# Kernel optimization log

Measured on AMD Instinct MI355X. Metric: run time of the kernel, lower is better.

## Reference

```python
import jax, jax.numpy as jnp
import numpy as np

DIM = 1024
HEADS = 16
SCALE = DIM ** (-0.5)  # NOTE: module scales by full dim, not head_dim


def setup_inputs() -> dict:
    key = jax.random.key(0)
    k1, k2, k3, k4 = jax.random.split(key, 4)
    x = jax.random.normal(k1, (4, 2048, DIM), dtype=jnp.float32)
    # torch Linear weights: y = x @ W.T
    w_qkv = jax.random.normal(k2, (3 * DIM, DIM), dtype=jnp.float32) * (DIM ** -0.5)
    w_out = jax.random.normal(k3, (DIM, DIM), dtype=jnp.float32) * (DIM ** -0.5)
    b_out = jax.random.normal(k4, (DIM,), dtype=jnp.float32) * 0.01
    return {"x": x, "w_qkv": w_qkv, "w_out": w_out, "b_out": b_out}


def reference(x, w_qkv, w_out, b_out):
    b, n, _ = x.shape
    h = HEADS
    d = DIM // h
    qkv = x @ w_qkv.T                                   # [b, n, 3*dim]
    qkv = qkv.reshape(b, n, 3, h, d)                    # split (qkv h d)
    qkv = jnp.transpose(qkv, (2, 0, 3, 1, 4))           # [3, b, h, n, d]
    q, k, v = qkv[0], qkv[1], qkv[2]
    dots = jnp.einsum('bhid,bhjd->bhij', q, k) * SCALE  # [b, h, n, n]
    attn = jax.nn.softmax(dots, axis=-1)
    out = jnp.einsum('bhij,bhjd->bhid', attn, v)        # [b, h, n, d]
    out = jnp.transpose(out, (0, 2, 1, 3)).reshape(b, n, h * d)
    return out @ w_out.T + b_out
```

## Files before the change

kernel.cpp:

```cpp
#include <hip/hip_runtime.h>

typedef short bf16x8 __attribute__((ext_vector_type(8)));
typedef float f32x4 __attribute__((ext_vector_type(4)));
typedef float f32x16 __attribute__((ext_vector_type(16)));

static __device__ __forceinline__ unsigned short f2bf(float f) {
  union { float f; unsigned u; } v; v.f = f;
  unsigned r = v.u + 0x7fffu + ((v.u >> 16) & 1u);
  return (unsigned short)(r >> 16);
}

static __device__ __forceinline__ unsigned pk2bf(float lo, float hi) {
  union { float f; unsigned u; } a, b; a.f = lo; b.f = hi;
  unsigned ra = a.u + 0x7fffu + ((a.u >> 16) & 1u);
  unsigned rb = b.u + 0x7fffu + ((b.u >> 16) & 1u);
  return __builtin_amdgcn_perm(rb, ra, 0x07060302);
}

static __device__ __forceinline__ void gll16(const unsigned short* g,
                                             unsigned short* l) {
  __builtin_amdgcn_global_load_lds(
      (const __attribute__((address_space(1))) unsigned int*)g,
      (__attribute__((address_space(3))) unsigned int*)l, 16, 0, 0);
}

__global__ void cvt_kernel(const float* __restrict__ src,
                           unsigned short* __restrict__ dst, int n4) {
  int i = blockIdx.x * blockDim.x + threadIdx.x;
  if (i >= n4) return;
  float4 f = ((const float4*)src)[i];
  ushort4 o;
  o.x = f2bf(f.x); o.y = f2bf(f.y); o.z = f2bf(f.z); o.w = f2bf(f.w);
  ((ushort4*)dst)[i] = o;
}

#define TM 128
#define TN 128
#define BK 64

template <int EPI>
__global__ __launch_bounds__(256, 2)
void gemm_bt(const unsigned short* __restrict__ X,
             const unsigned short* __restrict__ W,
             unsigned short* __restrict__ QKV, float* __restrict__ OUT,
             const float* __restrict__ bias, int M, int N, int K) {
  __shared__ __align__(16) unsigned short As[TM * BK];
  __shared__ __align__(16) unsigned short Bs[TN * BK];

  const int tid = threadIdx.x;
  const int lane = tid & 63;
  const int wave = tid >> 6;
  const int quad = lane >> 4;
  const int l16 = lane & 15;
  const int wm = wave >> 1, wn = wave & 1;

  const int m0 = blockIdx.y * TM;
  const int n0 = blockIdx.x * TN;

  const int sr = lane >> 3, sc = (lane & 7) * 8;

  f32x4 zero = {0.f, 0.f, 0.f, 0.f};
  f32x4 acc[4][4];
#pragma unroll
  for (int i = 0; i < 4; i++)
#pragma unroll
    for (int j = 0; j < 4; j++) acc[i][j] = zero;

  for (int k0 = 0; k0 < K; k0 += BK) {
    __syncthreads();
#pragma unroll
    for (int c = 0; c < 4; c++) {
      int row = wave * 32 + c * 8;
      gll16(&X[(size_t)(m0 + row + sr) * K + k0 + sc], &As[row * BK]);
      gll16(&W[(size_t)(n0 + row + sr) * K + k0 + sc], &Bs[row * BK]);
    }
    __syncthreads();
#pragma unroll
    for (int kk = 0; kk < 2; kk++) {
      bf16x8 af[4], bfr[4];
#pragma unroll
      for (int t = 0; t < 4; t++) {
        af[t]  = *(const bf16x8*)&As[(wm * 64 + t * 16 + l16) * BK + kk * 32 + quad * 8];
        bfr[t] = *(const bf16x8*)&Bs[(wn * 64 + t * 16 + l16) * BK + kk * 32 + quad * 8];
      }
#pragma unroll
      for (int mt = 0; mt < 4; mt++)
#pragma unroll
        for (int nt = 0; nt < 4; nt++)
          acc[mt][nt] = __builtin_amdgcn_mfma_f32_16x16x32_bf16(
              af[mt], bfr[nt], acc[mt][nt], 0, 0, 0);
    }
  }

#pragma unroll
  for (int mt = 0; mt < 4; mt++) {
#pragma unroll
    for (int nt = 0; nt < 4; nt++) {
      if (EPI == 0) {
        int nbase = n0 + wn * 64 + nt * 16;
        int which = nbase >> 10;
        if (which == 2) {
          int rem = (nbase + l16) & 1023;
          int h = rem >> 6, dd = rem & 63;
          int growb = m0 + wm * 64 + mt * 16 + quad * 4;
          int b = growb >> 11, nn0 = growb & 2047;
          ushort4 o;
          o.x = f2bf(acc[mt][nt][0]);
          o.y = f2bf(acc[mt][nt][1]);
          o.z = f2bf(acc[mt][nt][2]);
          o.w = f2bf(acc[mt][nt][3]);
          *(ushort4*)&QKV[16777216u + (((size_t)(b * 16 + h) * 64 + dd) << 11) + nn0] = o;
        } else {
#pragma unroll
          for (int r = 0; r < 4; r++) {
            int grow = m0 + wm * 64 + mt * 16 + quad * 4 + r;
            int gcol = nbase + l16;
            int rem = gcol & 1023;
            int h = rem >> 6, dd = rem & 63;
            float v = acc[mt][nt][r];
            if (which == 0) v *= 0.04508422f;
            int b = grow >> 11, nn = grow & 2047;
            QKV[(size_t)which * 8388608 +
                ((size_t)(b * 16 + h) * 2048 + nn) * 64 + dd] = f2bf(v);
          }
        }
      } else {
#pragma unroll
        for (int r = 0; r < 4; r++) {
          int grow = m0 + wm * 64 + mt * 16 + quad * 4 + r;
          int gcol = n0 + wn * 64 + nt * 16 + l16;
          OUT[(size_t)grow * N + gcol] = acc[mt][nt][r] + bias[gcol];
        }
      }
    }
  }
}

#define SK 72

__global__ __launch_bounds__(256, 2)
void attn_kernel(const unsigned short* __restrict__ Qg,
                 const unsigned short* __restrict__ Kg,
                 const unsigned short* __restrict__ Vg,
                 unsigned short* __restrict__ AO) {
  __shared__ __align__(16) unsigned short K_s[64 * SK];
  __shared__ __align__(16) unsigned short V_s[64 * SK];

  const int tid = threadIdx.x;
  const int lane = tid & 63;
  const int wave = tid >> 6;
  const int l31 = lane & 31;
  const int hh = lane >> 5;

  const int qb = blockIdx.x;
  const int bh = blockIdx.y;
  const size_t base = (size_t)bh * 131072;
  const int q0 = qb * 256 + wave * 64;

  bf16x8 bq[2][4];
#pragma unroll
  for (int mt = 0; mt < 2; mt++)
#pragma unroll
    for (int ks = 0; ks < 4; ks++)
      bq[mt][ks] = *(const bf16x8*)&Qg[base + (size_t)(q0 + mt * 32 + l31) * 64 +
                                       ks * 16 + hh * 8];

  f32x16 O[2][2];
#pragma unroll
  for (int mt = 0; mt < 2; mt++)
#pragma unroll
    for (int dt = 0; dt < 2; dt++)
#pragma unroll
      for (int r = 0; r < 16; r++) O[mt][dt][r] = 0.f;
  float lrow[2] = {0.f, 0.f};

  const int s_r = tid >> 3;
  const int s_c = (tid & 7) * 8;

  for (int j0 = 0; j0 < 2048; j0 += 64) {
    __syncthreads();
    *(uint4*)&K_s[s_r * SK + s_c] =
        *(const uint4*)&Kg[base + (size_t)(j0 + s_r) * 64 + s_c];
    *(uint4*)&K_s[(s_r + 32) * SK + s_c] =
        *(const uint4*)&Kg[base + (size_t)(j0 + s_r + 32) * 64 + s_c];
    *(uint4*)&V_s[s_r * SK + s_c] =
        *(const uint4*)&Vg[base + (size_t)s_r * 2048 + j0 + s_c];
    *(uint4*)&V_s[(s_r + 32) * SK + s_c] =
        *(const uint4*)&Vg[base + (size_t)(s_r + 32) * 2048 + j0 + s_c];
    __syncthreads();

    f32x16 S[2][2];
#pragma unroll
    for (int sub = 0; sub < 2; sub++) {
      f32x16 a0, a1;
#pragma unroll
      for (int r = 0; r < 16; r++) { a0[r] = 0.f; a1[r] = 0.f; }
#pragma unroll
      for (int ks = 0; ks < 4; ks++) {
        bf16x8 kf = *(const bf16x8*)&K_s[(sub * 32 + l31) * SK + ks * 16 + hh * 8];
        a0 = __builtin_amdgcn_mfma_f32_32x32x16_bf16(kf, bq[0][ks], a0, 0, 0, 0);
        a1 = __builtin_amdgcn_mfma_f32_32x32x16_bf16(kf, bq[1][ks], a1, 0, 0, 0);
      }
      S[sub][0] = a0; S[sub][1] = a1;
    }

#pragma unroll
    for (int mt = 0; mt < 2; mt++) {
      float rsum = 0.f;
#pragma unroll
      for (int sub = 0; sub < 2; sub++)
#pragma unroll
        for (int r = 0; r < 16; r++) {
          float p = __builtin_amdgcn_exp2f(S[sub][mt][r]);
          S[sub][mt][r] = p;
          rsum += p;
        }
      lrow[mt] += rsum;
    }

#pragma unroll
    for (int win = 0; win < 4; win++) {
      const int sub = win >> 1, kk = win & 1;
      const int g0 = kk * 2, g1 = kk * 2 + 1;
      bf16x8 pf[2];
#pragma unroll
      for (int mt = 0; mt < 2; mt++) {
        unsigned a00 = pk2bf(S[sub][mt][4 * g0 + 0], S[sub][mt][4 * g0 + 1]);
        unsigned a01 = pk2bf(S[sub][mt][4 * g0 + 2], S[sub][mt][4 * g0 + 3]);
        unsigned a10 = pk2bf(S[sub][mt][4 * g1 + 0], S[sub][mt][4 * g1 + 1]);
        unsigned a11 = pk2bf(S[sub][mt][4 * g1 + 2], S[sub][mt][4 * g1 + 3]);
        unsigned b00 = __shfl_xor((int)a00, 32);
        unsigned b01 = __shfl_xor((int)a01, 32);
        unsigned b10 = __shfl_xor((int)a10, 32);
        unsigned b11 = __shfl_xor((int)a11, 32);
        union { unsigned u[4]; bf16x8 v; } fr;
        fr.u[0] = hh ? b10 : a00;
        fr.u[1] = hh ? b11 : a01;
        fr.u[2] = hh ? a10 : b00;
        fr.u[3] = hh ? a11 : b01;
        pf[mt] = fr.v;
      }
#pragma unroll
      for (int dt = 0; dt < 2; dt++) {
        bf16x8 vf = *(const bf16x8*)&V_s[(dt * 32 + l31) * SK + win * 16 + hh * 8];
#pragma unroll
        for (int mt = 0; mt < 2; mt++)
          O[mt][dt] = __builtin_amdgcn_mfma_f32_32x32x16_bf16(vf, pf[mt], O[mt][dt], 0, 0, 0);
      }
    }
  }

  const int b4 = bh >> 4, head = bh & 15;
#pragma unroll
  for (int mt = 0; mt < 2; mt++) {
    lrow[mt] += __shfl_xor(lrow[mt], 32);
    float inv = 1.0f / lrow[mt];
    int row = b4 * 2048 + q0 + mt * 32 + l31;
#pragma unroll
    for (int dt = 0; dt < 2; dt++)
#pragma unroll
      for (int g = 0; g < 4; g++) {
        ushort4 o;
        o.x = f2bf(O[mt][dt][4 * g + 0] * inv);
        o.y = f2bf(O[mt][dt][4 * g + 1] * inv);
        o.z = f2bf(O[mt][dt][4 * g + 2] * inv);
        o.w = f2bf(O[mt][dt][4 * g + 3] * inv);
        *(ushort4*)&AO[(size_t)row * 1024 + head * 64 + dt * 32 + 8 * g + 4 * hh] = o;
      }
  }
}

extern "C" void kernel_launch(void* const* d_in, const int* in_sizes, int n_in,
                              void* d_out, int out_size, void* d_ws,
                              size_t ws_size, hipStream_t stream) {
  const float* x     = (const float*)d_in[0];
  const float* w_qkv = (const float*)d_in[1];
  const float* w_out = (const float*)d_in[2];
  const float* b_out = (const float*)d_in[3];
  float* out = (float*)d_out;

  unsigned short* ws = (unsigned short*)d_ws;
  unsigned short* Xbf  = ws;
  unsigned short* Wqkv = ws + 8388608;
  unsigned short* Wout = ws + 11534336;
  unsigned short* QKV  = ws + 12582912;
  unsigned short* AO   = ws;

  cvt_kernel<<<8192, 256, 0, stream>>>(x, Xbf, 2097152);
  cvt_kernel<<<3072, 256, 0, stream>>>(w_qkv, Wqkv, 786432);
  cvt_kernel<<<1024, 256, 0, stream>>>(w_out, Wout, 262144);

  gemm_bt<0><<<dim3(3072 / TN, 8192 / TM), 256, 0, stream>>>(
      Xbf, Wqkv, QKV, nullptr, nullptr, 8192, 3072, 1024);

  attn_kernel<<<dim3(8, 64), 256, 0, stream>>>(
      QKV, QKV + 8388608, QKV + 16777216, AO);

  gemm_bt<1><<<dim3(1024 / TN, 8192 / TM), 256, 0, stream>>>(
      AO, Wout, nullptr, out, b_out, 8192, 1024, 1024);
}
```

Measured before the change: 288.3 us.

## Swizzle LDS in GEMM and attention, double-buffer K/V with async loads

The GEMM's LDS tiles get an XOR column swizzle so that fragment reads spread across banks instead of conflicting. The attention kernel now double-buffers K/V tiles, filling them with global_load_lds prefetches of the next tile while the current one is computed. It also uses the same XOR swizzle in place of the padded layout. Each wave now owns 32 query rows instead of 64, the grid doubles and launch bounds ask for 4 blocks per CU, which raises occupancy but halves K/V reuse per block and doubles K/V global traffic. The loop keeps a single barrier per iteration; correctness depends on that barrier also covering completion of the previous async prefetch.

```diff
diff --git a/kernel.cpp b/kernel.cpp
--- a/kernel.cpp
+++ b/kernel.cpp
@@ -53,11 +53,13 @@
   const int quad = lane >> 4;
   const int l16 = lane & 15;
   const int wm = wave >> 1, wn = wave & 1;
+  const int rc = l16 & 7;
 
   const int m0 = blockIdx.y * TM;
   const int n0 = blockIdx.x * TN;
 
-  const int sr = lane >> 3, sc = (lane & 7) * 8;
+  const int sr = lane >> 3;
+  const int gsc = ((lane & 7) ^ sr) * 8;
 
   f32x4 zero = {0.f, 0.f, 0.f, 0.f};
   f32x4 acc[4][4];
@@ -71,17 +73,18 @@
 #pragma unroll
     for (int c = 0; c < 4; c++) {
       int row = wave * 32 + c * 8;
-      gll16(&X[(size_t)(m0 + row + sr) * K + k0 + sc], &As[row * BK]);
-      gll16(&W[(size_t)(n0 + row + sr) * K + k0 + sc], &Bs[row * BK]);
+      gll16(&X[(size_t)(m0 + row + sr) * K + k0 + gsc], &As[row * BK]);
+      gll16(&W[(size_t)(n0 + row + sr) * K + k0 + gsc], &Bs[row * BK]);
     }
     __syncthreads();
 #pragma unroll
     for (int kk = 0; kk < 2; kk++) {
       bf16x8 af[4], bfr[4];
+      const int csw = ((kk * 4 + quad) ^ rc) * 8;
 #pragma unroll
       for (int t = 0; t < 4; t++) {
-        af[t]  = *(const bf16x8*)&As[(wm * 64 + t * 16 + l16) * BK + kk * 32 + quad * 8];
-        bfr[t] = *(const bf16x8*)&Bs[(wn * 64 + t * 16 + l16) * BK + kk * 32 + quad * 8];
+        af[t]  = *(const bf16x8*)&As[(wm * 64 + t * 16 + l16) * BK + csw];
+        bfr[t] = *(const bf16x8*)&Bs[(wn * 64 + t * 16 + l16) * BK + csw];
       }
 #pragma unroll
       for (int mt = 0; mt < 4; mt++)
@@ -136,138 +139,128 @@
   }
 }
 
-#define SK 72
-
-__global__ __launch_bounds__(256, 2)
+__global__ __launch_bounds__(256, 4)
 void attn_kernel(const unsigned short* __restrict__ Qg,
                  const unsigned short* __restrict__ Kg,
                  const unsigned short* __restrict__ Vg,
                  unsigned short* __restrict__ AO) {
-  __shared__ __align__(16) unsigned short K_s[64 * SK];
-  __shared__ __align__(16) unsigned short V_s[64 * SK];
+  __shared__ __align__(16) unsigned short K_s[2][64 * 64];
+  __shared__ __align__(16) unsigned short V_s[2][64 * 64];
 
   const int tid = threadIdx.x;
   const int lane = tid & 63;
   const int wave = tid >> 6;
   const int l31 = lane & 31;
   const int hh = lane >> 5;
+  const int rc = l31 & 7;
 
   const int qb = blockIdx.x;
   const int bh = blockIdx.y;
   const size_t base = (size_t)bh * 131072;
-  const int q0 = qb * 256 + wave * 64;
-
-  bf16x8 bq[2][4];
-#pragma unroll
-  for (int mt = 0; mt < 2; mt++)
-#pragma unroll
-    for (int ks = 0; ks < 4; ks++)
-      bq[mt][ks] = *(const bf16x8*)&Qg[base + (size_t)(q0 + mt * 32 + l31) * 64 +
-                                       ks * 16 + hh * 8];
-
-  f32x16 O[2][2];
-#pragma unroll
-  for (int mt = 0; mt < 2; mt++)
-#pragma unroll
-    for (int dt = 0; dt < 2; dt++)
-#pragma unroll
-      for (int r = 0; r < 16; r++) O[mt][dt][r] = 0.f;
-  float lrow[2] = {0.f, 0.f};
-
-  const int s_r = tid >> 3;
-  const int s_c = (tid & 7) * 8;
-
-  for (int j0 = 0; j0 < 2048; j0 += 64) {
+  const int q0 = qb * 128 + wave * 32;
+
+  bf16x8 bq[4];
+#pragma unroll
+  for (int ks = 0; ks < 4; ks++)
+    bq[ks] = *(const bf16x8*)&Qg[base + (size_t)(q0 + l31) * 64 + ks * 16 + hh * 8];
+
+  f32x16 O[2];
+#pragma unroll
+  for (int dt = 0; dt < 2; dt++)
+#pragma unroll
+    for (int r = 0; r < 16; r++) O[dt][r] = 0.f;
+  float lrow = 0.f;
+
+  const int sr = lane >> 3;
+  const int gsc = ((lane & 7) ^ sr) * 8;
+  const unsigned short* Kb = Kg + base;
+  const unsigned short* Vb = Vg + base;
+
+#define PREFETCH(J0, B)                                                    \
+  {                                                                        \
+    _Pragma("unroll") for (int c = 0; c < 2; c++) {                        \
+      int r = wave * 16 + c * 8;                                           \
+      gll16(&Kb[(size_t)((J0) + r + sr) * 64 + gsc], &K_s[B][r * 64]);     \
+      gll16(&Vb[(size_t)(r + sr) * 2048 + (J0) + gsc], &V_s[B][r * 64]);   \
+    }                                                                      \
+  }
+
+  PREFETCH(0, 0);
+
+  for (int t = 0; t < 32; t++) {
     __syncthreads();
-    *(uint4*)&K_s[s_r * SK + s_c] =
-        *(const uint4*)&Kg[base + (size_t)(j0 + s_r) * 64 + s_c];
-    *(uint4*)&K_s[(s_r + 32) * SK + s_c] =
-        *(const uint4*)&Kg[base + (size_t)(j0 + s_r + 32) * 64 + s_c];
-    *(uint4*)&V_s[s_r * SK + s_c] =
-        *(const uint4*)&Vg[base + (size_t)s_r * 2048 + j0 + s_c];
-    *(uint4*)&V_s[(s_r + 32) * SK + s_c] =
-        *(const uint4*)&Vg[base + (size_t)(s_r + 32) * 2048 + j0 + s_c];
-    __syncthreads();
-
-    f32x16 S[2][2];
+    if (t < 31) PREFETCH((t + 1) * 64, (t + 1) & 1);
+    const unsigned short* Kc = K_s[t & 1];
+    const unsigned short* Vc = V_s[t & 1];
+
+    f32x16 S[2];
 #pragma unroll
     for (int sub = 0; sub < 2; sub++) {
-      f32x16 a0, a1;
-#pragma unroll
-      for (int r = 0; r < 16; r++) { a0[r] = 0.f; a1[r] = 0.f; }
+      f32x16 a;
+#pragma unroll
+      for (int r = 0; r < 16; r++) a[r] = 0.f;
 #pragma unroll
       for (int ks = 0; ks < 4; ks++) {
-        bf16x8 kf = *(const bf16x8*)&K_s[(sub * 32 + l31) * SK + ks * 16 + hh * 8];
-        a0 = __builtin_amdgcn_mfma_f32_32x32x16_bf16(kf, bq[0][ks], a0, 0, 0, 0);
-        a1 = __builtin_amdgcn_mfma_f32_32x32x16_bf16(kf, bq[1][ks], a1, 0, 0, 0);
-      }
-      S[sub][0] = a0; S[sub][1] = a1;
-    }
-
-#pragma unroll
-    for (int mt = 0; mt < 2; mt++) {
-      float rsum = 0.f;
-#pragma unroll
-      for (int sub = 0; sub < 2; sub++)
-#pragma unroll
-        for (int r = 0; r < 16; r++) {
-          float p = __builtin_amdgcn_exp2f(S[sub][mt][r]);
-          S[sub][mt][r] = p;
-          rsum += p;
-        }
-      lrow[mt] += rsum;
-    }
+        bf16x8 kf = *(const bf16x8*)&Kc[(sub * 32 + l31) * 64 +
+                                        (((ks * 2 + hh) ^ rc) * 8)];
+        a = __builtin_amdgcn_mfma_f32_32x32x16_bf16(kf, bq[ks], a, 0, 0, 0);
+      }
+      S[sub] = a;
+    }
+
+    float rsum = 0.f;
+#pragma unroll
+    for (int sub = 0; sub < 2; sub++)
+#pragma unroll
+      for (int r = 0; r < 16; r++) {
+        float p = __builtin_amdgcn_exp2f(S[sub][r]);
+        S[sub][r] = p;
+        rsum += p;
+      }
+    lrow += rsum;
 
 #pragma unroll
     for (int win = 0; win < 4; win++) {
       const int sub = win >> 1, kk = win & 1;
       const int g0 = kk * 2, g1 = kk * 2 + 1;
-      bf16x8 pf[2];
-#pragma unroll
-      for (int mt = 0; mt < 2; mt++) {
-        unsigned a00 = pk2bf(S[sub][mt][4 * g0 + 0], S[sub][mt][4 * g0 + 1]);
-        unsigned a01 = pk2bf(S[sub][mt][4 * g0 + 2], S[sub][mt][4 * g0 + 3]);
-        unsigned a10 = pk2bf(S[sub][mt][4 * g1 + 0], S[sub][mt][4 * g1 + 1]);
-        unsigned a11 = pk2bf(S[sub][mt][4 * g1 + 2], S[sub][mt][4 * g1 + 3]);
-        unsigned b00 = __shfl_xor((int)a00, 32);
-        unsigned b01 = __shfl_xor((int)a01, 32);
-        unsigned b10 = __shfl_xor((int)a10, 32);
-        unsigned b11 = __shfl_xor((int)a11, 32);
-        union { unsigned u[4]; bf16x8 v; } fr;
-        fr.u[0] = hh ? b10 : a00;
-        fr.u[1] = hh ? b11 : a01;
-        fr.u[2] = hh ? a10 : b00;
-        fr.u[3] = hh ? a11 : b01;
-        pf[mt] = fr.v;
-      }
+      unsigned a00 = pk2bf(S[sub][4 * g0 + 0], S[sub][4 * g0 + 1]);
+      unsigned a01 = pk2bf(S[sub][4 * g0 + 2], S[sub][4 * g0 + 3]);
+      unsigned a10 = pk2bf(S[sub][4 * g1 + 0], S[sub][4 * g1 + 1]);
+      unsigned a11 = pk2bf(S[sub][4 * g1 + 2], S[sub][4 * g1 + 3]);
+      unsigned b00 = __shfl_xor((int)a00, 32);
+      unsigned b01 = __shfl_xor((int)a01, 32);
+      unsigned b10 = __shfl_xor((int)a10, 32);
+      unsigned b11 = __shfl_xor((int)a11, 32);
+      union { unsigned u[4]; bf16x8 v; } fr;
+      fr.u[0] = hh ? b10 : a00;
+      fr.u[1] = hh ? b11 : a01;
+      fr.u[2] = hh ? a10 : b00;
+      fr.u[3] = hh ? a11 : b01;
+      bf16x8 pf = fr.v;
 #pragma unroll
       for (int dt = 0; dt < 2; dt++) {
-        bf16x8 vf = *(const bf16x8*)&V_s[(dt * 32 + l31) * SK + win * 16 + hh * 8];
-#pragma unroll
-        for (int mt = 0; mt < 2; mt++)
-          O[mt][dt] = __builtin_amdgcn_mfma_f32_32x32x16_bf16(vf, pf[mt], O[mt][dt], 0, 0, 0);
+        bf16x8 vf = *(const bf16x8*)&Vc[(dt * 32 + l31) * 64 +
+                                        (((win * 2 + hh) ^ rc) * 8)];
+        O[dt] = __builtin_amdgcn_mfma_f32_32x32x16_bf16(vf, pf, O[dt], 0, 0, 0);
       }
     }
   }
 
   const int b4 = bh >> 4, head = bh & 15;
-#pragma unroll
-  for (int mt = 0; mt < 2; mt++) {
-    lrow[mt] += __shfl_xor(lrow[mt], 32);
-    float inv = 1.0f / lrow[mt];
-    int row = b4 * 2048 + q0 + mt * 32 + l31;
-#pragma unroll
-    for (int dt = 0; dt < 2; dt++)
-#pragma unroll
-      for (int g = 0; g < 4; g++) {
-        ushort4 o;
-        o.x = f2bf(O[mt][dt][4 * g + 0] * inv);
-        o.y = f2bf(O[mt][dt][4 * g + 1] * inv);
-        o.z = f2bf(O[mt][dt][4 * g + 2] * inv);
-        o.w = f2bf(O[mt][dt][4 * g + 3] * inv);
-        *(ushort4*)&AO[(size_t)row * 1024 + head * 64 + dt * 32 + 8 * g + 4 * hh] = o;
-      }
-  }
+  lrow += __shfl_xor(lrow, 32);
+  float inv = 1.0f / lrow;
+  int row = b4 * 2048 + q0 + l31;
+#pragma unroll
+  for (int dt = 0; dt < 2; dt++)
+#pragma unroll
+    for (int g = 0; g < 4; g++) {
+      ushort4 o;
+      o.x = f2bf(O[dt][4 * g + 0] * inv);
+      o.y = f2bf(O[dt][4 * g + 1] * inv);
+      o.z = f2bf(O[dt][4 * g + 2] * inv);
+      o.w = f2bf(O[dt][4 * g + 3] * inv);
+      *(ushort4*)&AO[(size_t)row * 1024 + head * 64 + dt * 32 + 8 * g + 4 * hh] = o;
+    }
 }
 
 extern "C" void kernel_launch(void* const* d_in, const int* in_sizes, int n_in,
@@ -293,7 +286,7 @@
   gemm_bt<0><<<dim3(3072 / TN, 8192 / TM), 256, 0, stream>>>(
       Xbf, Wqkv, QKV, nullptr, nullptr, 8192, 3072, 1024);
 
-  attn_kernel<<<dim3(8, 64), 256, 0, stream>>>(
+  attn_kernel<<<dim3(16, 64), 256, 0, stream>>>(
       QKV, QKV + 8388608, QKV + 16777216, AO);
 
   gemm_bt<1><<<dim3(1024 / TN, 8192 / TM), 256, 0, stream>>>(
```

Result: faster. 278.7 us (-3.3%).
